# Kernel optimization log

Measured on AMD Instinct MI355X. Metric: run time of the kernel, lower is better.

The kernel has to match this reference:

```python
import jax, jax.numpy as jnp
import numpy as np

N = 500000   # num instances
C = 64       # num clock regions (8x8 grid)
CHIP_W, CHIP_H = 168.0, 480.0


def setup_inputs() -> dict:
    key = jax.random.key(0)
    k1, k2, k3 = jax.random.split(key, 3)
    # 8x8 grid of clock-region well boxes (xl, yl, xh, yh) tiling the chip
    gx, gy = 8, 8
    cw, ch = CHIP_W / gx, CHIP_H / gy
    ix = np.arange(C) % gx
    iy = np.arange(C) // gx
    well_boxes = jnp.asarray(
        np.stack([ix * cw, iy * ch, (ix + 1) * cw, (iy + 1) * ch], axis=1),
        dtype=jnp.float32)
    # instance centers uniformly over the chip
    inst_pos = jax.random.uniform(k1, (N, 2), dtype=jnp.float32) * jnp.array(
        [CHIP_W, CHIP_H], dtype=jnp.float32)
    # half sizes in [0.25, 0.75) sites (module stores inst_sizes * 0.5)
    half_inst_sizes = jax.random.uniform(k2, (N, 2), dtype=jnp.float32) * 0.5 + 0.25
    inst_areas = 4.0 * half_inst_sizes[:, 0] * half_inst_sizes[:, 1]
    # per-instance candidate CR availability; guarantee >=1 available CR
    avail = jax.random.randint(k3, (N, C), 0, 2) > 0
    avail = avail.at[:, 0].set(True)
    exponents = jnp.full((N,), 2.0, dtype=jnp.float32)
    return {
        'inst_pos': inst_pos,
        'half_inst_sizes': half_inst_sizes,
        'inst_areas': inst_areas,
        'well_boxes': well_boxes,
        'inst_cr_avail_map': avail,
        'exponents': exponents,
    }


def reference(inst_pos, half_inst_sizes, inst_areas, well_boxes,
              inst_cr_avail_map, exponents):
    # Per-instance CR selection + box-overlap well energy.
    x = inst_pos[:, 0:1]           # (N,1)
    y = inst_pos[:, 1:2]
    hx = half_inst_sizes[:, 0:1]
    hy = half_inst_sizes[:, 1:2]
    xl, yl, xh, yh = (well_boxes[:, 0], well_boxes[:, 1],
                      well_boxes[:, 2], well_boxes[:, 3])  # each (C,)
    # protrusion distance of the instance box outside each well box, (N,C)
    dx = jnp.maximum(jnp.maximum(xl - (x - hx), (x + hx) - xh), 0.0)
    dy = jnp.maximum(jnp.maximum(yl - (y - hy), (y + hy) - yh), 0.0)
    dist = dx + dy
    # mask out unavailable clock regions, pick nearest available CR
    dist = jnp.where(inst_cr_avail_map, dist, jnp.inf)
    selected_crs = jnp.argmin(dist, axis=1)  # (N,)
    dx_sel = jnp.take_along_axis(dx, selected_crs[:, None], axis=1)[:, 0]
    dy_sel = jnp.take_along_axis(dy, selected_crs[:, None], axis=1)[:, 0]
    # per-instance exponentiated well energy
    energy = jnp.power(dx_sel, exponents) + jnp.power(dy_sel, exponents)
    return energy
```

## Files before the change

kernel.cpp:

```cpp
#include <hip/hip_runtime.h>
#include <stdint.h>


#define C_WELLS 64

template <int CTRL>
__device__ __forceinline__ unsigned long long dpp64(unsigned long long k) {
    int lo = (int)(unsigned)k;
    int hi = (int)(unsigned)(k >> 32);
    lo = __builtin_amdgcn_update_dpp(0, lo, CTRL, 0xF, 0xF, true);
    hi = __builtin_amdgcn_update_dpp(0, hi, CTRL, 0xF, 0xF, true);
    return ((unsigned long long)(unsigned)hi << 32) | (unsigned)lo;
}

__device__ __forceinline__ unsigned long long umin64(unsigned long long a,
                                                     unsigned long long b) {
    return a < b ? a : b;
}

__global__ __launch_bounds__(256, 6)
void energy_well_kernel(const float2* __restrict__ inst_pos,
                        const float2* __restrict__ half_sizes,
                        const float*  __restrict__ well_boxes,
                        const int4*   __restrict__ avail4,
                        const float*  __restrict__ exponents,
                        float* __restrict__ out,
                        int N, int nT16)
{
    const int lane = threadIdx.x & 63;
    const int sub  = lane & 3;
    const int tile = (int)((blockIdx.x * blockDim.x + threadIdx.x) >> 6);
    if (tile >= nT16) return;

    const int i  = tile * 16 + (lane >> 2);
    const int ii = i < N ? i : N - 1;

    const int4* a = avail4 + ((size_t)ii * 16 + (size_t)sub * 4);
    const int4 av0 = a[0], av1 = a[1], av2 = a[2], av3 = a[3];
    const float2 p = inst_pos[ii];
    const float2 h = half_sizes[ii];
    const float  e = exponents[ii];

    float xlv[8], xhv[8];
    #pragma unroll
    for (int ix = 0; ix < 8; ++ix) {
        xlv[ix] = well_boxes[4 * ix + 0];
        xhv[ix] = well_boxes[4 * ix + 2];
    }
    const float ylA = well_boxes[64 * sub + 1];
    const float yhA = well_boxes[64 * sub + 3];
    const float ylB = well_boxes[64 * sub + 33];
    const float yhB = well_boxes[64 * sub + 35];

    const float xm = p.x - h.x, xp_ = p.x + h.x;
    const float ym = p.y - h.y, yp_ = p.y + h.y;

    float dxv[8];
    #pragma unroll
    for (int ix = 0; ix < 8; ++ix)
        dxv[ix] = fmaxf(fmaxf(xlv[ix] - xm, xp_ - xhv[ix]), 0.0f);
    const float dyA = fmaxf(fmaxf(ylA - ym, yp_ - yhA), 0.0f);
    const float dyB = fmaxf(fmaxf(ylB - ym, yp_ - yhB), 0.0f);

    const unsigned gbase = (unsigned)(sub << 4);
    unsigned long long gm[4];
    #pragma unroll
    for (int j = 0; j < 4; ++j) {
        const int4 a4 = (j == 0) ? av0 : (j == 1) ? av1 : (j == 2) ? av2 : av3;
        unsigned long long acc = ~0ull;
        #pragma unroll
        for (int k = 0; k < 4; ++k) {
            const int c2 = 4 * j + k;
            const int avw = (k == 0) ? a4.x : (k == 1) ? a4.y
                          : (k == 2) ? a4.z : a4.w;
            const float dy   = (c2 < 8) ? dyA : dyB;
            const float dist = dxv[c2 & 7] + dy;
            unsigned long long key =
                (((unsigned long long)__float_as_uint(dist)) << 6)
                | (unsigned long long)(gbase + (unsigned)c2);
            key = avw ? key : ~0ull;
            acc = umin64(acc, key);
        }
        gm[j] = acc;
    }
    unsigned long long kmin = umin64(umin64(gm[0], gm[1]), umin64(gm[2], gm[3]));

    kmin = umin64(kmin, dpp64<0xB1>(kmin));
    kmin = umin64(kmin, dpp64<0x4E>(kmin));

    const int g = (int)(kmin & 63);
    const int s = g & 7;
    float a0 = (s & 1) ? dxv[1] : dxv[0];
    float a1 = (s & 1) ? dxv[3] : dxv[2];
    float a2 = (s & 1) ? dxv[5] : dxv[4];
    float a3 = (s & 1) ? dxv[7] : dxv[6];
    float b0 = (s & 2) ? a1 : a0;
    float b1 = (s & 2) ? a3 : a2;
    const float dxs = (s & 4) ? b1 : b0;
    const float dys = (g & 8) ? dyB : dyA;

    if (((g >> 4) == sub) && (i < N)) {
        float energy;
        if (e == 2.0f) energy = dxs * dxs + dys * dys;
        else           energy = powf(dxs, e) + powf(dys, e);
        out[i] = energy;
    }
}

extern "C" void kernel_launch(void* const* d_in, const int* in_sizes, int n_in,
                              void* d_out, int out_size, void* d_ws, size_t ws_size,
                              hipStream_t stream)
{
    const float2* inst_pos   = (const float2*)d_in[0];
    const float2* half_sizes = (const float2*)d_in[1];
    const float*  well_boxes = (const float*)d_in[3];
    const int4*   avail4     = (const int4*)d_in[4];
    const float*  exponents  = (const float*)d_in[5];
    float* out = (float*)d_out;

    const int N = in_sizes[5];
    const int nT16 = (N + 15) / 16;
    const int blocks = (nT16 + 3) / 4;

    energy_well_kernel<<<dim3(blocks), dim3(256), 0, stream>>>(
        inst_pos, half_sizes, well_boxes, avail4, exponents, out, N, nT16);
}
```

Measured before the change: 196.3 us.

## Remap lanes to 16-lane rows per instance with coalesced avail loads and float DPP argmin

Reassigns work so each instance is handled by a 16-lane row, each lane covering 4 clock regions, instead of 4 lanes covering 16 each. Avail-map loads become fully coalesced contiguous int4 reads across the wavefront. The 64-bit packed key min is replaced by a float min via row_shr DPP steps plus a ballot to find the first matching lane, which keeps argmin tie-breaking on the lowest index. Each thread now processes 4 instances sequentially, which adds DPP, ballot and per-instance load overhead, and the row_shr reduction's correctness depends on only the last lane of each row reading the full minimum.

```diff
diff --git a/kernel.cpp b/kernel.cpp
--- a/kernel.cpp
+++ b/kernel.cpp
@@ -5,17 +5,10 @@
 #define C_WELLS 64
 
 template <int CTRL>
-__device__ __forceinline__ unsigned long long dpp64(unsigned long long k) {
-    int lo = (int)(unsigned)k;
-    int hi = (int)(unsigned)(k >> 32);
-    lo = __builtin_amdgcn_update_dpp(0, lo, CTRL, 0xF, 0xF, true);
-    hi = __builtin_amdgcn_update_dpp(0, hi, CTRL, 0xF, 0xF, true);
-    return ((unsigned long long)(unsigned)hi << 32) | (unsigned)lo;
-}
-
-__device__ __forceinline__ unsigned long long umin64(unsigned long long a,
-                                                     unsigned long long b) {
-    return a < b ? a : b;
+__device__ __forceinline__ float fmin_dpp(float v) {
+    const float o = __uint_as_float(__builtin_amdgcn_update_dpp(
+        0, (int)__float_as_uint(v), CTRL, 0xF, 0xF, true));
+    return fminf(v, o);
 }
 
 __global__ __launch_bounds__(256, 6)
@@ -28,18 +21,32 @@
                         int N, int nT16)
 {
     const int lane = threadIdx.x & 63;
-    const int sub  = lane & 3;
+    const int q    = lane & 15;
+    const int g    = lane >> 4;
     const int tile = (int)((blockIdx.x * blockDim.x + threadIdx.x) >> 6);
     if (tile >= nT16) return;
+    const int base = tile << 4;
 
-    const int i  = tile * 16 + (lane >> 2);
-    const int ii = i < N ? i : N - 1;
-
-    const int4* a = avail4 + ((size_t)ii * 16 + (size_t)sub * 4);
-    const int4 av0 = a[0], av1 = a[1], av2 = a[2], av3 = a[3];
-    const float2 p = inst_pos[ii];
-    const float2 h = half_sizes[ii];
-    const float  e = exponents[ii];
+    const size_t idx0 = (size_t)tile * 256 + (size_t)lane;
+    const size_t last = (size_t)N * 16 - 1;
+    int4 av[4];
+    #pragma unroll
+    for (int j = 0; j < 4; ++j) {
+        const size_t idx = idx0 + (size_t)(64 * j);
+        av[j] = avail4[idx <= last ? idx : last];
+    }
+    float2 pj[4], hj[4]; float ej[4];
+    #pragma unroll
+    for (int j = 0; j < 4; ++j) {
+        const int i  = base + 4 * j + g;
+        const int ii = i < N ? i : N - 1;
+        pj[j] = inst_pos[ii];
+        hj[j] = half_sizes[ii];
+        ej[j] = exponents[ii];
+    }
+    const int iy = q >> 1;
+    const float ylq = well_boxes[32 * iy + 1];
+    const float yhq = well_boxes[32 * iy + 3];
 
     float xlv[8], xhv[8];
     #pragma unroll
@@ -47,63 +54,54 @@
         xlv[ix] = well_boxes[4 * ix + 0];
         xhv[ix] = well_boxes[4 * ix + 2];
     }
-    const float ylA = well_boxes[64 * sub + 1];
-    const float yhA = well_boxes[64 * sub + 3];
-    const float ylB = well_boxes[64 * sub + 33];
-    const float yhB = well_boxes[64 * sub + 35];
+    const bool hiHalf = (q & 1) != 0;
+    float xlq[4], xhq[4];
+    #pragma unroll
+    for (int t = 0; t < 4; ++t) {
+        xlq[t] = hiHalf ? xlv[4 + t] : xlv[t];
+        xhq[t] = hiHalf ? xhv[4 + t] : xhv[t];
+    }
 
-    const float xm = p.x - h.x, xp_ = p.x + h.x;
-    const float ym = p.y - h.y, yp_ = p.y + h.y;
-
-    float dxv[8];
-    #pragma unroll
-    for (int ix = 0; ix < 8; ++ix)
-        dxv[ix] = fmaxf(fmaxf(xlv[ix] - xm, xp_ - xhv[ix]), 0.0f);
-    const float dyA = fmaxf(fmaxf(ylA - ym, yp_ - yhA), 0.0f);
-    const float dyB = fmaxf(fmaxf(ylB - ym, yp_ - yhB), 0.0f);
-
-    const unsigned gbase = (unsigned)(sub << 4);
-    unsigned long long gm[4];
     #pragma unroll
     for (int j = 0; j < 4; ++j) {
-        const int4 a4 = (j == 0) ? av0 : (j == 1) ? av1 : (j == 2) ? av2 : av3;
-        unsigned long long acc = ~0ull;
+        const int i = base + 4 * j + g;
+        const float xm = pj[j].x - hj[j].x, xp_ = pj[j].x + hj[j].x;
+        const float ym = pj[j].y - hj[j].y, yp_ = pj[j].y + hj[j].y;
+        const float dy = fmaxf(fmaxf(ylq - ym, yp_ - yhq), 0.0f);
+
+        const int4 a4 = av[j];
+        float dx[4], dist[4];
         #pragma unroll
-        for (int k = 0; k < 4; ++k) {
-            const int c2 = 4 * j + k;
-            const int avw = (k == 0) ? a4.x : (k == 1) ? a4.y
-                          : (k == 2) ? a4.z : a4.w;
-            const float dy   = (c2 < 8) ? dyA : dyB;
-            const float dist = dxv[c2 & 7] + dy;
-            unsigned long long key =
-                (((unsigned long long)__float_as_uint(dist)) << 6)
-                | (unsigned long long)(gbase + (unsigned)c2);
-            key = avw ? key : ~0ull;
-            acc = umin64(acc, key);
+        for (int t = 0; t < 4; ++t) {
+            dx[t] = fmaxf(fmaxf(xlq[t] - xm, xp_ - xhq[t]), 0.0f);
+            const int avw = (t == 0) ? a4.x : (t == 1) ? a4.y
+                          : (t == 2) ? a4.z : a4.w;
+            dist[t] = avw ? (dx[t] + dy) : __builtin_inff();
         }
-        gm[j] = acc;
-    }
-    unsigned long long kmin = umin64(umin64(gm[0], gm[1]), umin64(gm[2], gm[3]));
+        const float lmin = fminf(fminf(dist[0], dist[1]),
+                                 fminf(dist[2], dist[3]));
 
-    kmin = umin64(kmin, dpp64<0xB1>(kmin));
-    kmin = umin64(kmin, dpp64<0x4E>(kmin));
+        float rmin = lmin;
+        rmin = fmin_dpp<0x121>(rmin);
+        rmin = fmin_dpp<0x122>(rmin);
+        rmin = fmin_dpp<0x124>(rmin);
+        rmin = fmin_dpp<0x128>(rmin);
 
-    const int g = (int)(kmin & 63);
-    const int s = g & 7;
-    float a0 = (s & 1) ? dxv[1] : dxv[0];
-    float a1 = (s & 1) ? dxv[3] : dxv[2];
-    float a2 = (s & 1) ? dxv[5] : dxv[4];
-    float a3 = (s & 1) ? dxv[7] : dxv[6];
-    float b0 = (s & 2) ? a1 : a0;
-    float b1 = (s & 2) ? a3 : a2;
-    const float dxs = (s & 4) ? b1 : b0;
-    const float dys = (g & 8) ? dyB : dyA;
+        const unsigned long long b = __ballot(lmin == rmin);
+        const unsigned rowmask = (unsigned)((b >> (lane & 48)) & 0xFFFFull);
+        const int wq = __ffs(rowmask) - 1;
 
-    if (((g >> 4) == sub) && (i < N)) {
-        float energy;
-        if (e == 2.0f) energy = dxs * dxs + dys * dys;
-        else           energy = powf(dxs, e) + powf(dys, e);
-        out[i] = energy;
+        if ((q == wq) && (i < N)) {
+            float dxs = dx[3];
+            dxs = (dist[2] == rmin) ? dx[2] : dxs;
+            dxs = (dist[1] == rmin) ? dx[1] : dxs;
+            dxs = (dist[0] == rmin) ? dx[0] : dxs;
+            const float e = ej[j];
+            float energy;
+            if (e == 2.0f) energy = dxs * dxs + dy * dy;
+            else           energy = powf(dxs, e) + powf(dy, e);
+            out[i] = energy;
+        }
     }
 }
 
```

New measurement: 203.9 us. 3.8% more time.
